# Optimization experiments

Measured on AMD Instinct MI355X. Metric: run time of the kernel, lower is better.

Reference implementation:

```python
import jax, jax.numpy as jnp
import numpy as np

B, S, D, QD, OUT = 32, 2048, 768, 256, 1024

def setup_inputs() -> dict:
    key = jax.random.key(0)
    k = jax.random.split(key, 8)
    data = jax.random.normal(k[0], (B, S, D), dtype=jnp.float32)
    seq_len = jax.random.randint(k[1], (B,), 0, S)
    # learned params (Linear: y = x @ W.T + b)
    s1 = 1.0 / np.sqrt(D)
    s3 = 1.0 / np.sqrt(QD)
    W1 = jax.random.uniform(k[2], (QD, D), minval=-s1, maxval=s1, dtype=jnp.float32)
    b1 = jax.random.uniform(k[3], (QD,), minval=-s1, maxval=s1, dtype=jnp.float32)
    W2 = jax.random.uniform(k[4], (QD, D), minval=-s1, maxval=s1, dtype=jnp.float32)
    b2 = jax.random.uniform(k[5], (QD,), minval=-s1, maxval=s1, dtype=jnp.float32)
    W3 = jax.random.uniform(k[6], (OUT, QD), minval=-s3, maxval=s3, dtype=jnp.float32)
    b3 = jax.random.uniform(k[7], (OUT,), minval=-s3, maxval=s3, dtype=jnp.float32)
    return {"data": data, "seq_len": seq_len, "W1": W1, "b1": b1,
            "W2": W2, "b2": b2, "W3": W3, "b3": b3}

def reference(data, seq_len, W1, b1, W2, b2, W3, b3):
    # Q, K projections: [B,S,QD]
    Q = jnp.einsum('bsd,qd->bsq', data, W1) + b1
    K = jnp.einsum('bsd,qd->bsq', data, W2) + b2
    # scores = K @ Q^T / sqrt(QD): [B,S,S]
    scores = jnp.einsum('biq,bjq->bij', K, Q) / np.sqrt(QD).astype(np.float32)
    attn = jax.nn.softmax(scores, axis=2)
    # attention output uses K as values: [B,S,QD]
    x = jnp.einsum('bij,bjq->biq', attn, K)
    # max-pool over sequence dim -> [B,QD]
    x = jnp.max(x, axis=1)
    out = jax.nn.relu(jnp.einsum('bq,oq->bo', x, W3) + b3)
    return out
```

## Files before the change

kernel.cpp:

```cpp
#include <hip/hip_runtime.h>
#include <hip/hip_bf16.h>

#define Bn   32
#define Sn   2048
#define Dn   768
#define QDn  256
#define OUTn 1024

typedef __attribute__((ext_vector_type(8))) short          bf16x8;
typedef __attribute__((ext_vector_type(4))) float          f32x4;
typedef __attribute__((ext_vector_type(8))) unsigned short u16x8;
typedef __attribute__((ext_vector_type(4))) unsigned short u16x4;

typedef unsigned short ushort_t;

__device__ __forceinline__ unsigned short f2bf(float f) {
    unsigned int u = __float_as_uint(f);
    u = (u + 0x7FFFu + ((u >> 16) & 1u)) >> 16;
    return (unsigned short)u;
}
#define MFMA16(a,b,c) __builtin_amdgcn_mfma_f32_16x16x32_bf16((a),(b),(c),0,0,0)

__global__ __launch_bounds__(256) void wconv_kernel(
    const float* __restrict__ W1, const float* __restrict__ W2,
    ushort_t* __restrict__ W1h, ushort_t* __restrict__ W2h)
{
    const int idx = blockIdx.x * 256 + threadIdx.x;
    W1h[idx] = f2bf(W1[idx]);
    W2h[idx] = f2bf(W2[idx]);
}

__global__ __launch_bounds__(256, 2) void proj_kernel(
    const float* __restrict__ data,
    const ushort_t* __restrict__ W1h, const float* __restrict__ b1,
    const ushort_t* __restrict__ W2h, const float* __restrict__ b2,
    ushort_t* __restrict__ Qb, ushort_t* __restrict__ Kb,
    ushort_t* __restrict__ KTb)
{
    __shared__ __align__(16) char smem[34816];
    ushort_t* DH = (ushort_t*)smem;
    ushort_t* WH = (ushort_t*)(smem + 10240);
    ushort_t* EP = (ushort_t*)smem;

    const int tid  = threadIdx.x;
    const int w    = tid >> 6;
    const int quad = (tid >> 4) & 3;
    const int n15  = tid & 15;
    const int mtile = blockIdx.y;
    const int half  = blockIdx.x;
    const bool isQ  = (half == 0);
    const ushort_t* WhP = isQ ? W1h : W2h;
    const float* bp = isQ ? b1 : b2;

    f32x4 acc[2][16];
    #pragma unroll
    for (int i = 0; i < 2; ++i)
        #pragma unroll
        for (int j = 0; j < 16; ++j) acc[i][j] = (f32x4)0.f;

    const size_t drow = (size_t)mtile * 128;

    for (int kt = 0; kt < 24; ++kt) {
        const int kc = kt * 32;
        {
            const int m  = tid >> 1;
            const int k0 = (tid & 1) << 4;
            const float* src = data + (drow + m) * 768 + kc + k0;
            const float4 v0 = *(const float4*)(src);
            const float4 v1 = *(const float4*)(src + 4);
            const float4 v2 = *(const float4*)(src + 8);
            const float4 v3 = *(const float4*)(src + 12);
            u16x8 h0, h1;
            h0[0]=f2bf(v0.x); h0[1]=f2bf(v0.y); h0[2]=f2bf(v0.z); h0[3]=f2bf(v0.w);
            h0[4]=f2bf(v1.x); h0[5]=f2bf(v1.y); h0[6]=f2bf(v1.z); h0[7]=f2bf(v1.w);
            h1[0]=f2bf(v2.x); h1[1]=f2bf(v2.y); h1[2]=f2bf(v2.z); h1[3]=f2bf(v2.w);
            h1[4]=f2bf(v3.x); h1[5]=f2bf(v3.y); h1[6]=f2bf(v3.z); h1[7]=f2bf(v3.w);
            *(u16x8*)&DH[m*40 + k0]     = h0;
            *(u16x8*)&DH[m*40 + k0 + 8] = h1;
        }
        #pragma unroll
        for (int u = 0; u < 4; ++u) {
            const int nrow = (tid >> 2) + u * 64;
            const int ko   = (tid & 3) << 3;
            *(u16x8*)&WH[nrow*40 + ko] = *(const u16x8*)(WhP + (size_t)nrow * 768 + kc + ko);
        }
        __syncthreads();
        bf16x8 ah[2];
        #pragma unroll
        for (int ms = 0; ms < 2; ++ms)
            ah[ms] = *(bf16x8*)&DH[(w*32 + ms*16 + n15)*40 + quad*8];
        #pragma unroll
        for (int ns = 0; ns < 16; ++ns) {
            const bf16x8 bh = *(bf16x8*)&WH[(ns*16 + n15)*40 + quad*8];
            #pragma unroll
            for (int ms = 0; ms < 2; ++ms)
                acc[ms][ns] = MFMA16(ah[ms], bh, acc[ms][ns]);
        }
        __syncthreads();
    }

    float bv[16];
    #pragma unroll
    for (int ns = 0; ns < 16; ++ns) bv[ns] = bp[ns*16 + n15];

    {
        ushort_t* dstRM = isQ ? Qb : Kb;
        #pragma unroll
        for (int hf = 0; hf < 2; ++hf) {
            __syncthreads();
            if ((w >> 1) == hf) {
                #pragma unroll
                for (int ms = 0; ms < 2; ++ms)
                    #pragma unroll
                    for (int ns = 0; ns < 16; ++ns)
                        #pragma unroll
                        for (int r = 0; r < 4; ++r) {
                            const int rl = (w & 1)*32 + ms*16 + quad*4 + r;
                            EP[rl*264 + ns*16 + n15] = f2bf(acc[ms][ns][r] + bv[ns]);
                        }
            }
            __syncthreads();
            const int row = tid >> 2;
            #pragma unroll
            for (int u = 0; u < 8; ++u) {
                const int co = (tid & 3)*8 + u*32;
                *(u16x8*)(dstRM + (drow + hf*64 + row)*256 + co) =
                    *(u16x8*)&EP[row*264 + co];
            }
        }
    }
    if (!isQ) {
        const int bidx = mtile >> 4;
        const int s0   = (mtile & 15) * 128;
        #pragma unroll
        for (int qh = 0; qh < 2; ++qh) {
            __syncthreads();
            #pragma unroll
            for (int ms = 0; ms < 2; ++ms)
                #pragma unroll
                for (int ns8 = 0; ns8 < 8; ++ns8) {
                    const int ns = qh*8 + ns8;
                    #pragma unroll
                    for (int r = 0; r < 4; ++r) {
                        const int rowm = w*32 + ms*16 + quad*4 + r;
                        EP[(ns8*16 + n15)*136 + rowm] = f2bf(acc[ms][ns][r] + bv[ns]);
                    }
                }
            __syncthreads();
            const int q = tid >> 1;
            #pragma unroll
            for (int u = 0; u < 8; ++u) {
                const int mo = (tid & 1)*8 + u*16;
                *(u16x8*)(KTb + ((size_t)(bidx*256 + qh*128 + q))*2048 + s0 + mo) =
                    *(u16x8*)&EP[q*136 + mo];
            }
        }
    }
}

__global__ __launch_bounds__(256, 2) void attn_kernel(
    const ushort_t* __restrict__ Qb, const ushort_t* __restrict__ Kb,
    const ushort_t* __restrict__ KTb, float* __restrict__ pmax)
{
    __shared__ __align__(16) char smem[73728];
    ushort_t* QS  = (ushort_t*)smem;
    ushort_t* KTS = (ushort_t*)(smem + 17408);
    ushort_t* PS  = (ushort_t*)(smem + 54272);
    float*    l_lds = (float*)(smem + 72704);

    const int tid  = threadIdx.x;
    const int w    = tid >> 6;
    const int quad = (tid >> 4) & 3;
    const int n15  = tid & 15;
    const int b    = blockIdx.x;
    const int it   = blockIdx.y;
    const int i0   = it * 128;

    const ushort_t* QbB  = Qb  + (size_t)b * Sn * QDn;
    const ushort_t* KbB  = Kb  + (size_t)b * Sn * QDn;
    const ushort_t* KTbB = KTb + (size_t)b * QDn * Sn;

    bf16x8 kf[2][8];
    #pragma unroll
    for (int isub = 0; isub < 2; ++isub) {
        const size_t irow = (size_t)(i0 + w*32 + isub*16 + n15) * QDn;
        #pragma unroll
        for (int ks = 0; ks < 8; ++ks)
            kf[isub][ks] = *(const bf16x8*)(KbB + irow + ks*32 + quad*8);
    }

    f32x4 xq[4][8];
    #pragma unroll
    for (int qs = 0; qs < 4; ++qs)
        #pragma unroll
        for (int is = 0; is < 8; ++is) xq[qs][is] = (f32x4)0.f;
    float l_i[2] = {0.f, 0.f};

    for (int jt = 0; jt < Sn; jt += 64) {
        __syncthreads();
        {
            const int j = tid >> 2;
            const int c = (tid & 3) * 32;
            const ushort_t* src = QbB + (size_t)(jt + j) * QDn + c;
            #pragma unroll
            for (int u = 0; u < 4; ++u)
                *(u16x8*)&QS[j*136 + c + u*8] = *(const u16x8*)(src + u*8);
        }
        {
            const int joff = (tid & 7) * 8;
            #pragma unroll
            for (int p = 0; p < 8; ++p) {
                const int q = (tid >> 3) + p*32;
                *(u16x8*)&KTS[q*72 + joff] =
                    *(const u16x8*)(KTbB + (size_t)q * Sn + jt + joff);
            }
        }
        __syncthreads();
        f32x4 sc[4][2];
        #pragma unroll
        for (int js = 0; js < 4; ++js) { sc[js][0] = (f32x4)0.f; sc[js][1] = (f32x4)0.f; }
        #pragma unroll
        for (int ks = 0; ks < 4; ++ks) {
            #pragma unroll
            for (int js = 0; js < 4; ++js) {
                const bf16x8 ah = *(bf16x8*)&QS[(js*16 + n15)*136 + ks*32 + quad*8];
                sc[js][0] = MFMA16(ah, kf[0][ks], sc[js][0]);
                sc[js][1] = MFMA16(ah, kf[1][ks], sc[js][1]);
            }
        }
        __syncthreads();
        {
            const int j = tid >> 2;
            const int c = (tid & 3) * 32;
            const ushort_t* src = QbB + (size_t)(jt + j) * QDn + 128 + c;
            #pragma unroll
            for (int u = 0; u < 4; ++u)
                *(u16x8*)&QS[j*136 + c + u*8] = *(const u16x8*)(src + u*8);
        }
        __syncthreads();
        #pragma unroll
        for (int ks = 4; ks < 8; ++ks) {
            #pragma unroll
            for (int js = 0; js < 4; ++js) {
                const bf16x8 ah = *(bf16x8*)&QS[(js*16 + n15)*136 + (ks & 3)*32 + quad*8];
                sc[js][0] = MFMA16(ah, kf[0][ks], sc[js][0]);
                sc[js][1] = MFMA16(ah, kf[1][ks], sc[js][1]);
            }
        }
        #pragma unroll
        for (int isub = 0; isub < 2; ++isub) {
            const int prow = (isub*16 + w*32 + n15) * 72;
            float rs = 0.f;
            #pragma unroll
            for (int js = 0; js < 4; ++js) {
                u16x4 ph;
                #pragma unroll
                for (int r = 0; r < 4; ++r) {
                    const float p = __expf(sc[js][isub][r] * 0.0625f);
                    rs += p;
                    ph[r] = f2bf(p);
                }
                *(u16x4*)&PS[prow + js*16 + quad*4] = ph;
            }
            rs += __shfl_xor(rs, 16, 64);
            rs += __shfl_xor(rs, 32, 64);
            l_i[isub] += rs;
        }
        __syncthreads();
        #pragma unroll
        for (int ks2 = 0; ks2 < 2; ++ks2) {
            bf16x8 at[4];
            #pragma unroll
            for (int qs = 0; qs < 4; ++qs)
                at[qs] = *(bf16x8*)&KTS[(w*64 + qs*16 + n15)*72 + ks2*32 + quad*8];
            #pragma unroll
            for (int is = 0; is < 8; ++is) {
                const bf16x8 pb = *(bf16x8*)&PS[(is*16 + n15)*72 + ks2*32 + quad*8];
                #pragma unroll
                for (int qs = 0; qs < 4; ++qs)
                    xq[qs][is] = MFMA16(at[qs], pb, xq[qs][is]);
            }
        }
    }

    __syncthreads();
    if (quad == 0) {
        l_lds[w*32 + n15]      = l_i[0];
        l_lds[w*32 + 16 + n15] = l_i[1];
    }
    __syncthreads();
    float linv[8];
    #pragma unroll
    for (int is = 0; is < 8; ++is) linv[is] = 1.0f / l_lds[is*16 + n15];
    #pragma unroll
    for (int qs = 0; qs < 4; ++qs) {
        #pragma unroll
        for (int r = 0; r < 4; ++r) {
            float mv = xq[qs][0][r] * linv[0];
            #pragma unroll
            for (int is = 1; is < 8; ++is)
                mv = fmaxf(mv, xq[qs][is][r] * linv[is]);
            mv = fmaxf(mv, __shfl_xor(mv, 1, 64));
            mv = fmaxf(mv, __shfl_xor(mv, 2, 64));
            mv = fmaxf(mv, __shfl_xor(mv, 4, 64));
            mv = fmaxf(mv, __shfl_xor(mv, 8, 64));
            if (n15 == 0) {
                const int q = w*64 + qs*16 + quad*4 + r;
                pmax[((size_t)b * 16 + it) * QDn + q] = mv;
            }
        }
    }
}

__global__ __launch_bounds__(256) void head_kernel(
    const float* __restrict__ pmax,
    const float* __restrict__ W3, const float* __restrict__ b3,
    float* __restrict__ out)
{
    __shared__ float xs[QDn];
    const int b = blockIdx.x, tid = threadIdx.x;
    float m = pmax[((size_t)b * 16) * QDn + tid];
    #pragma unroll
    for (int t = 1; t < 16; ++t)
        m = fmaxf(m, pmax[((size_t)b * 16 + t) * QDn + tid]);
    xs[tid] = m;
    __syncthreads();
    #pragma unroll
    for (int u = 0; u < 4; ++u) {
        const int o = (u << 8) + tid;
        const float4* wv = (const float4*)(W3 + (size_t)o * QDn);
        float s = 0.f;
        #pragma unroll 8
        for (int q4 = 0; q4 < QDn / 4; ++q4) {
            const float4 w4 = wv[q4];
            const float4 x4 = *(const float4*)&xs[q4 << 2];
            s += w4.x * x4.x + w4.y * x4.y + w4.z * x4.z + w4.w * x4.w;
        }
        out[(size_t)b * OUTn + o] = fmaxf(s + b3[o], 0.f);
    }
}

extern "C" void kernel_launch(void* const* d_in, const int* in_sizes, int n_in,
                              void* d_out, int out_size, void* d_ws, size_t ws_size,
                              hipStream_t stream) {
    const float* data = (const float*)d_in[0];
    const float* W1 = (const float*)d_in[2];
    const float* b1 = (const float*)d_in[3];
    const float* W2 = (const float*)d_in[4];
    const float* b2 = (const float*)d_in[5];
    const float* W3 = (const float*)d_in[6];
    const float* b3 = (const float*)d_in[7];
    float* out = (float*)d_out;

    ushort_t* Qb  = (ushort_t*)d_ws;
    ushort_t* Kb  = Qb  + 16777216;
    ushort_t* KTb = Kb  + 16777216;
    float*    pmax = (float*)((char*)d_ws + 100663296);
    ushort_t* W1h = (ushort_t*)((char*)d_ws + 100663296 + 524288);
    ushort_t* W2h = W1h + 196608;

    wconv_kernel<<<768, 256, 0, stream>>>(W1, W2, W1h, W2h);
    dim3 gP(2, 512);
    proj_kernel<<<gP, 256, 0, stream>>>(data, W1h, b1, W2h, b2, Qb, Kb, KTb);
    dim3 gA(Bn, 16);
    attn_kernel<<<gA, 256, 0, stream>>>(Qb, Kb, KTb, pmax);
    head_kernel<<<Bn, 256, 0, stream>>>(pmax, W3, b3, out);
}
```

Before: 696.5 us.

## Stage full Q tile with XOR swizzle, load K^T directly into registers

The attention loop now stages the entire 64x256 Q tile in LDS at once, using an XOR-swizzled layout instead of padding. This removes the second half-tile reload and its two extra barriers per iteration. The K^T tile is no longer staged in LDS: each wave loads its own 64 rows straight from global memory into registers before the PV MFMAs, and the P buffer also moves to the swizzled layout. LDS use shrinks, but register pressure rises and K^T reads now go to global/L2 without LDS sharing.

```diff
diff --git a/kernel.cpp b/kernel.cpp
--- a/kernel.cpp
+++ b/kernel.cpp
@@ -162,11 +162,10 @@
     const ushort_t* __restrict__ Qb, const ushort_t* __restrict__ Kb,
     const ushort_t* __restrict__ KTb, float* __restrict__ pmax)
 {
-    __shared__ __align__(16) char smem[73728];
-    ushort_t* QS  = (ushort_t*)smem;
-    ushort_t* KTS = (ushort_t*)(smem + 17408);
-    ushort_t* PS  = (ushort_t*)(smem + 54272);
-    float*    l_lds = (float*)(smem + 72704);
+    __shared__ __align__(16) char smem[49664];
+    ushort_t* QS = (ushort_t*)smem;
+    ushort_t* PS = (ushort_t*)(smem + 32768);
+    float*    l_lds = (float*)(smem + 49152);
 
     const int tid  = threadIdx.x;
     const int w    = tid >> 6;
@@ -196,23 +195,19 @@
         for (int is = 0; is < 8; ++is) xq[qs][is] = (f32x4)0.f;
     float l_i[2] = {0.f, 0.f};
 
+    const int swz  = (n15 & 7) * 8;
+    const int jrow = tid >> 2;
+    const int wsw  = (jrow & 7) * 8;
+
     for (int jt = 0; jt < Sn; jt += 64) {
         __syncthreads();
         {
-            const int j = tid >> 2;
-            const int c = (tid & 3) * 32;
-            const ushort_t* src = QbB + (size_t)(jt + j) * QDn + c;
-            #pragma unroll
-            for (int u = 0; u < 4; ++u)
-                *(u16x8*)&QS[j*136 + c + u*8] = *(const u16x8*)(src + u*8);
-        }
-        {
-            const int joff = (tid & 7) * 8;
-            #pragma unroll
-            for (int p = 0; p < 8; ++p) {
-                const int q = (tid >> 3) + p*32;
-                *(u16x8*)&KTS[q*72 + joff] =
-                    *(const u16x8*)(KTbB + (size_t)q * Sn + jt + joff);
+            const ushort_t* src = QbB + (size_t)(jt + jrow) * QDn + (tid & 3) * 64;
+            ushort_t* dst = QS + jrow * 256;
+            #pragma unroll
+            for (int u = 0; u < 8; ++u) {
+                const int col = (tid & 3) * 64 + u * 8;
+                *(u16x8*)&dst[col ^ wsw] = *(const u16x8*)(src + u * 8);
             }
         }
         __syncthreads();
@@ -220,36 +215,17 @@
         #pragma unroll
         for (int js = 0; js < 4; ++js) { sc[js][0] = (f32x4)0.f; sc[js][1] = (f32x4)0.f; }
         #pragma unroll
-        for (int ks = 0; ks < 4; ++ks) {
+        for (int ks = 0; ks < 8; ++ks) {
             #pragma unroll
             for (int js = 0; js < 4; ++js) {
-                const bf16x8 ah = *(bf16x8*)&QS[(js*16 + n15)*136 + ks*32 + quad*8];
+                const bf16x8 ah = *(bf16x8*)&QS[(js*16 + n15)*256 + ((ks*32 + quad*8) ^ swz)];
                 sc[js][0] = MFMA16(ah, kf[0][ks], sc[js][0]);
                 sc[js][1] = MFMA16(ah, kf[1][ks], sc[js][1]);
             }
         }
-        __syncthreads();
-        {
-            const int j = tid >> 2;
-            const int c = (tid & 3) * 32;
-            const ushort_t* src = QbB + (size_t)(jt + j) * QDn + 128 + c;
-            #pragma unroll
-            for (int u = 0; u < 4; ++u)
-                *(u16x8*)&QS[j*136 + c + u*8] = *(const u16x8*)(src + u*8);
-        }
-        __syncthreads();
-        #pragma unroll
-        for (int ks = 4; ks < 8; ++ks) {
-            #pragma unroll
-            for (int js = 0; js < 4; ++js) {
-                const bf16x8 ah = *(bf16x8*)&QS[(js*16 + n15)*136 + (ks & 3)*32 + quad*8];
-                sc[js][0] = MFMA16(ah, kf[0][ks], sc[js][0]);
-                sc[js][1] = MFMA16(ah, kf[1][ks], sc[js][1]);
-            }
-        }
         #pragma unroll
         for (int isub = 0; isub < 2; ++isub) {
-            const int prow = (isub*16 + w*32 + n15) * 72;
+            const int prow = (w*32 + isub*16 + n15) * 64;
             float rs = 0.f;
             #pragma unroll
             for (int js = 0; js < 4; ++js) {
@@ -260,25 +236,28 @@
                     rs += p;
                     ph[r] = f2bf(p);
                 }
-                *(u16x4*)&PS[prow + js*16 + quad*4] = ph;
+                *(u16x4*)&PS[prow + ((js*16 + quad*4) ^ swz)] = ph;
             }
             rs += __shfl_xor(rs, 16, 64);
             rs += __shfl_xor(rs, 32, 64);
             l_i[isub] += rs;
         }
+        bf16x8 at2[2][4];
+        #pragma unroll
+        for (int ks2 = 0; ks2 < 2; ++ks2)
+            #pragma unroll
+            for (int qs = 0; qs < 4; ++qs)
+                at2[ks2][qs] = *(const bf16x8*)(
+                    KTbB + (size_t)(w*64 + qs*16 + n15) * Sn + jt + ks2*32 + quad*8);
         __syncthreads();
         #pragma unroll
         for (int ks2 = 0; ks2 < 2; ++ks2) {
-            bf16x8 at[4];
-            #pragma unroll
-            for (int qs = 0; qs < 4; ++qs)
-                at[qs] = *(bf16x8*)&KTS[(w*64 + qs*16 + n15)*72 + ks2*32 + quad*8];
             #pragma unroll
             for (int is = 0; is < 8; ++is) {
-                const bf16x8 pb = *(bf16x8*)&PS[(is*16 + n15)*72 + ks2*32 + quad*8];
+                const bf16x8 pb = *(bf16x8*)&PS[(is*16 + n15)*64 + ((ks2*32 + quad*8) ^ swz)];
                 #pragma unroll
                 for (int qs = 0; qs < 4; ++qs)
-                    xq[qs][is] = MFMA16(at[qs], pb, xq[qs][is]);
+                    xq[qs][is] = MFMA16(at2[ks2][qs], pb, xq[qs][is]);
             }
         }
     }
```

After: 663.9 us. 1.05x faster.
